# Optimization experiments

Hardware: AMD Instinct MI355X
Metric: run time of the kernel (lower is better)

Reference implementation:

```python
import jax, jax.numpy as jnp
import numpy as np

N = 100_000   # nodes
E = 1_250_000 # edges
D = 64        # feature dim


def setup_inputs() -> dict:
    key = jax.random.key(0)
    k1, k2, k3, k4 = jax.random.split(key, 4)
    x = jax.random.normal(k1, (N, D), dtype=jnp.float32)
    edge_index = jax.random.randint(k2, (2, E), 0, N, dtype=jnp.int32)
    s = 1.0 / np.sqrt(D)  # glorot-ish scale
    W1 = jax.random.uniform(k3, (D, D), minval=-s, maxval=s, dtype=jnp.float32)
    W2 = jax.random.uniform(k4, (D, D), minval=-s, maxval=s, dtype=jnp.float32)
    b1 = jnp.zeros((D,), jnp.float32)
    b2 = jnp.zeros((D,), jnp.float32)
    return {"x": x, "edge_index": edge_index, "W1": W1, "b1": b1, "W2": W2, "b2": b2}


def gcn_conv(x, edge_index, W, b):
    # PyG GCNConv: add self-loops, symmetric normalization D^-1/2 A D^-1/2,
    # linear transform, scatter-add aggregation over destination nodes.
    n = x.shape[0]
    src, dst = edge_index[0], edge_index[1]
    xw = x @ W  # [N, D]
    deg = jax.ops.segment_sum(jnp.ones((edge_index.shape[1],), x.dtype), dst,
                              num_segments=n) + 1.0  # +1 for self-loop
    inv_sqrt = jax.lax.rsqrt(deg)  # [N]
    coef = inv_sqrt[src] * inv_sqrt[dst]  # [E]
    agg = jax.ops.segment_sum(xw[src] * coef[:, None], dst, num_segments=n)
    # self-loop contribution: coef_ii = deg_i^-1
    agg = agg + xw * (inv_sqrt * inv_sqrt)[:, None]
    return agg + b


def reference(x, edge_index, W1, b1, W2, b2):
    h = jax.nn.relu(gcn_conv(x, edge_index, W1, b1))
    # dropout p=0.6 is identity in eval mode (training=False)
    out = gcn_conv(h, edge_index, W2, b2)
    return jax.nn.log_softmax(out, axis=1)
```

## Files before the change

kernel.cpp:

```cpp
#include <hip/hip_runtime.h>

#define DD 64
#define BSH 8
#define NB_MAX 512
#define SCAP 4096
#define BIN_CH 4096

typedef __attribute__((ext_vector_type(8))) short bf16x8;
typedef __attribute__((ext_vector_type(4))) float f32x4;
union Frag { bf16x8 v; uint32_t d[4]; };

__device__ __forceinline__ float bf_lo(uint32_t d) { return __uint_as_float(d << 16); }
__device__ __forceinline__ float bf_hi(uint32_t d) { return __uint_as_float(d & 0xffff0000u); }
__device__ __forceinline__ float bf2f(uint32_t h) { return __uint_as_float(h << 16); }
__device__ __forceinline__ uint32_t f2bf(float f) {
    uint32_t u = __float_as_uint(f);
    u += 0x7fffu + ((u >> 16) & 1u);
    return u >> 16;
}

__global__ __launch_bounds__(256) void bin_kernel(const int* __restrict__ src,
                                                  const int* __restrict__ dst,
                                                  int* __restrict__ bcnt,
                                                  uint32_t* __restrict__ staging,
                                                  int E, int NB) {
    __shared__ uint32_t cnt[NB_MAX];
    __shared__ uint32_t resv[NB_MAX];
    __shared__ uint16_t rk[BIN_CH];
    int tid = threadIdx.x;
    int base = blockIdx.x * BIN_CH;
    for (int b = tid; b < NB; b += 256) cnt[b] = 0;
    __syncthreads();
    for (int k = tid; k < BIN_CH; k += 256) {
        int g = base + k;
        if (g < E) {
            int b = dst[g] >> BSH;
            rk[k] = (uint16_t)atomicAdd(&cnt[b], 1u);
        }
    }
    __syncthreads();
    for (int b = tid; b < NB; b += 256) {
        uint32_t c = cnt[b];
        resv[b] = c ? (uint32_t)atomicAdd(&bcnt[b], (int)c) : 0u;
    }
    __syncthreads();
    for (int k = tid; k < BIN_CH; k += 256) {
        int g = base + k;
        if (g < E) {
            int s = src[g], d = dst[g];
            int b = d >> BSH;
            uint32_t pos = resv[b] + rk[k];
            if (pos < SCAP)
                staging[(size_t)b * SCAP + pos] = ((uint32_t)s << BSH) | (uint32_t)(d & ((1 << BSH) - 1));
        }
    }
}

__global__ __launch_bounds__(256) void sort_kernel(const int* __restrict__ bcnt,
                                                   const uint32_t* __restrict__ staging,
                                                   int* __restrict__ rowptr,
                                                   float* __restrict__ inv,
                                                   uint32_t* __restrict__ srcs,
                                                   int n, int E, int NB) {
    __shared__ uint32_t raw[SCAP];
    __shared__ uint32_t sorted[SCAP];
    __shared__ int scnt[1 << BSH];
    __shared__ int soff[1 << BSH];
    __shared__ int lcur[1 << BSH];
    __shared__ int red[256];
    int tid = threadIdx.x;
    int b = blockIdx.x;
    int base = b << BSH;
    int nd = min(1 << BSH, n - base);
    int cb = min(bcnt[b], SCAP);

    int part = 0;
    for (int j = tid; j < b; j += 256) part += bcnt[j];
    red[tid] = part;
    __syncthreads();
    for (int o = 128; o > 0; o >>= 1) {
        if (tid < o) red[tid] += red[tid + o];
        __syncthreads();
    }
    int bbase = red[0];

    scnt[tid] = 0;
    if (tid < ((1 << BSH) - 256)) {}
    __syncthreads();
    for (int k = tid; k < cb; k += 256) {
        uint32_t w = staging[(size_t)b * SCAP + k];
        raw[k] = w;
        atomicAdd(&scnt[w & ((1 << BSH) - 1)], 1);
    }
    __syncthreads();
    int v = scnt[tid];
    red[tid] = v;
    __syncthreads();
    for (int o = 1; o < 256; o <<= 1) {
        int t = (tid >= o) ? red[tid - o] : 0;
        __syncthreads();
        red[tid] += t;
        __syncthreads();
    }
    soff[tid] = red[tid] - v;
    lcur[tid] = red[tid] - v;
    if (tid < nd) {
        rowptr[base + tid] = bbase + soff[tid];
        inv[base + tid] = rsqrtf((float)v + 1.0f);
    }
    if (b == NB - 1 && tid == 0) rowptr[n] = E;
    __syncthreads();
    for (int k = tid; k < cb; k += 256) {
        uint32_t w = raw[k];
        int p = atomicAdd(&lcur[w & ((1 << BSH) - 1)], 1);
        sorted[p] = w >> BSH;
    }
    __syncthreads();
    for (int k = tid; k < cb; k += 256) srcs[bbase + k] = sorted[k];
}

template <int XBF>
__global__ __launch_bounds__(256) void gemm64_mfma(const void* __restrict__ Xv,
                                                   const float* __restrict__ W,
                                                   uint16_t* __restrict__ Y, int n) {
    __shared__ float Ws[DD * DD];
    int tid = threadIdx.x;
    for (int i = tid; i < DD * DD; i += 256) Ws[i] = W[i];
    __syncthreads();
    int lane = tid & 63, quad = lane >> 4, l16 = lane & 15;

    Frag bhi[4][2], blo[4][2];
#pragma unroll
    for (int t = 0; t < 4; ++t)
#pragma unroll
        for (int c = 0; c < 2; ++c) {
            int col = t * 16 + l16;
            int kb = c * 32 + quad * 8;
#pragma unroll
            for (int i = 0; i < 4; ++i) {
                float w0 = Ws[(kb + 2 * i) * DD + col];
                float w1 = Ws[(kb + 2 * i + 1) * DD + col];
                uint32_t h0 = f2bf(w0), h1 = f2bf(w1);
                uint32_t l0 = f2bf(w0 - bf2f(h0)), l1 = f2bf(w1 - bf2f(h1));
                bhi[t][c].d[i] = h0 | (h1 << 16);
                blo[t][c].d[i] = l0 | (l1 << 16);
            }
        }

    int ngroups = (n + 15) >> 4;
    int nwaves = gridDim.x * 4;
    int wid = blockIdx.x * 4 + (tid >> 6);
    for (int g = wid; g < ngroups; g += nwaves) {
        int rb = g << 4;
        int row = min(rb + l16, n - 1);
        f32x4 acc[4];
#pragma unroll
        for (int t = 0; t < 4; ++t) acc[t] = (f32x4){0.f, 0.f, 0.f, 0.f};
#pragma unroll
        for (int c = 0; c < 2; ++c) {
            Frag ahi, alo;
            if constexpr (XBF == 0) {
                const float* xr = (const float*)Xv + (size_t)row * DD + c * 32 + quad * 8;
                float4 x0 = *(const float4*)xr;
                float4 x1 = *(const float4*)(xr + 4);
                float f[8] = {x0.x, x0.y, x0.z, x0.w, x1.x, x1.y, x1.z, x1.w};
#pragma unroll
                for (int i = 0; i < 4; ++i) {
                    uint32_t h0 = f2bf(f[2 * i]), h1 = f2bf(f[2 * i + 1]);
                    ahi.d[i] = h0 | (h1 << 16);
                    alo.d[i] = f2bf(f[2 * i] - bf2f(h0)) | (f2bf(f[2 * i + 1] - bf2f(h1)) << 16);
                }
            } else {
                const int4* xr = (const int4*)((const uint32_t*)Xv + (size_t)row * 32 + c * 16 + quad * 4);
                int4 a = *xr;
                ahi.d[0] = a.x; ahi.d[1] = a.y; ahi.d[2] = a.z; ahi.d[3] = a.w;
            }
#pragma unroll
            for (int t = 0; t < 4; ++t) {
                acc[t] = __builtin_amdgcn_mfma_f32_16x16x32_bf16(ahi.v, bhi[t][c].v, acc[t], 0, 0, 0);
                acc[t] = __builtin_amdgcn_mfma_f32_16x16x32_bf16(ahi.v, blo[t][c].v, acc[t], 0, 0, 0);
                if constexpr (XBF == 0)
                    acc[t] = __builtin_amdgcn_mfma_f32_16x16x32_bf16(alo.v, bhi[t][c].v, acc[t], 0, 0, 0);
            }
        }
#pragma unroll
        for (int t = 0; t < 4; ++t)
#pragma unroll
            for (int r = 0; r < 4; ++r) {
                int ro = rb + quad * 4 + r;
                if (ro < n) Y[(size_t)ro * DD + t * 16 + l16] = (uint16_t)f2bf(acc[t][r]);
            }
    }
}

template <int MODE>
__global__ __launch_bounds__(256) void agg_kernel(const int* __restrict__ rowptr,
                                                  const uint32_t* __restrict__ srcs,
                                                  const float* __restrict__ inv,
                                                  const uint32_t* __restrict__ XWb,
                                                  const float* __restrict__ b,
                                                  void* __restrict__ OUTv, int n) {
    int gid = blockIdx.x * 256 + threadIdx.x;
    int i = gid >> 6, lane = gid & 63;
    if (i >= n) return;
    int q = lane >> 4, m = lane & 15;

    float iv = inv[i];
    float a0 = 0.f, a1 = 0.f, a2 = 0.f, a3 = 0.f;
    if (q == 0) {
        float iv2 = iv * iv;
        int2 d = *(const int2*)(XWb + (size_t)i * 32 + 2 * m);
        float4 bb = *(const float4*)(b + 4 * m);
        a0 = fmaf(bf_lo((uint32_t)d.x), iv2, bb.x);
        a1 = fmaf(bf_hi((uint32_t)d.x), iv2, bb.y);
        a2 = fmaf(bf_lo((uint32_t)d.y), iv2, bb.z);
        a3 = fmaf(bf_hi((uint32_t)d.y), iv2, bb.w);
    }

    int jstart = rowptr[i], jend = rowptr[i + 1];
    if (jstart < jend) {
        int last = jend - 1;
        int jq = jstart + q;
        uint32_t s0 = srcs[min(jq, last)];
        uint32_t s1 = srcs[min(jq + 4, last)];
        uint32_t s2 = srcs[min(jq + 8, last)];
        float v0 = inv[s0], v1 = inv[s1];
        int2 d0 = *(const int2*)(XWb + (size_t)s0 * 32 + 2 * m);
        int2 d1 = *(const int2*)(XWb + (size_t)s1 * 32 + 2 * m);
        for (int j = jq; j < jend; j += 4) {
            uint32_t s3 = srcs[min(j + 12, last)];
            float v2 = inv[s2];
            int2 d2 = *(const int2*)(XWb + (size_t)s2 * 32 + 2 * m);
            float c = v0 * iv;
            a0 = fmaf(bf_lo((uint32_t)d0.x), c, a0);
            a1 = fmaf(bf_hi((uint32_t)d0.x), c, a1);
            a2 = fmaf(bf_lo((uint32_t)d0.y), c, a2);
            a3 = fmaf(bf_hi((uint32_t)d0.y), c, a3);
            s0 = s1; s1 = s2; s2 = s3;
            v0 = v1; v1 = v2;
            d0 = d1; d1 = d2;
        }
    }

    a0 += __shfl_xor(a0, 32, 64); a0 += __shfl_xor(a0, 16, 64);
    a1 += __shfl_xor(a1, 32, 64); a1 += __shfl_xor(a1, 16, 64);
    a2 += __shfl_xor(a2, 32, 64); a2 += __shfl_xor(a2, 16, 64);
    a3 += __shfl_xor(a3, 32, 64); a3 += __shfl_xor(a3, 16, 64);

    if (MODE == 0) {
        if (q == 0) {
            int2 d;
            d.x = (int)((f2bf(fmaxf(a1, 0.f)) << 16) | f2bf(fmaxf(a0, 0.f)));
            d.y = (int)((f2bf(fmaxf(a3, 0.f)) << 16) | f2bf(fmaxf(a2, 0.f)));
            *(int2*)((uint32_t*)OUTv + (size_t)i * 32 + 2 * m) = d;
        }
    } else {
        float mx = fmaxf(fmaxf(a0, a1), fmaxf(a2, a3));
#pragma unroll
        for (int o = 8; o > 0; o >>= 1) mx = fmaxf(mx, __shfl_xor(mx, o, 64));
        float e = __expf(a0 - mx) + __expf(a1 - mx) + __expf(a2 - mx) + __expf(a3 - mx);
#pragma unroll
        for (int o = 8; o > 0; o >>= 1) e += __shfl_xor(e, o, 64);
        float ls = __logf(e);
        if (q == 0) {
            float4 r = make_float4(a0 - mx - ls, a1 - mx - ls, a2 - mx - ls, a3 - mx - ls);
            *(float4*)((float*)OUTv + (size_t)i * DD + 4 * m) = r;
        }
    }
}

extern "C" void kernel_launch(void* const* d_in, const int* in_sizes, int n_in,
                              void* d_out, int out_size, void* d_ws, size_t ws_size,
                              hipStream_t stream) {
    const float* x  = (const float*)d_in[0];
    const int*   ei = (const int*)d_in[1];
    const float* W1 = (const float*)d_in[2];
    const float* b1 = (const float*)d_in[3];
    const float* W2 = (const float*)d_in[4];
    const float* b2 = (const float*)d_in[5];
    float* out = (float*)d_out;

    const int n = in_sizes[0] / DD;
    const int E = in_sizes[1] / 2;
    const int* src = ei;
    const int* dst = ei + E;
    const int NB = (n + (1 << BSH) - 1) >> BSH;

    size_t off = 0;
    int* base = (int*)d_ws;
    int* bcnt = base + off; off += NB_MAX;
    uint32_t* staging = (uint32_t*)(base + off); off += (size_t)NB_MAX * SCAP;
    uint32_t* srcs = (uint32_t*)(base + off); off += E;
    int* rowptr = base + off; off += (size_t)n + 1;
    float* inv  = (float*)(base + off); off += n;
    uint32_t* XWb = (uint32_t*)(base + off); off += (size_t)n * 32;
    uint32_t* hb  = (uint32_t*)(base + off); off += (size_t)n * 32;

    hipMemsetAsync(bcnt, 0, NB_MAX * sizeof(int), stream);
    bin_kernel<<<(E + BIN_CH - 1) / BIN_CH, 256, 0, stream>>>(src, dst, bcnt, staging, E, NB);
    sort_kernel<<<NB, 256, 0, stream>>>(bcnt, staging, rowptr, inv, srcs, n, E, NB);

    gemm64_mfma<0><<<1024, 256, 0, stream>>>(x, W1, (uint16_t*)XWb, n);
    agg_kernel<0><<<(n * DD + 255) / 256, 256, 0, stream>>>(rowptr, srcs, inv, XWb, b1, hb, n);

    gemm64_mfma<1><<<1024, 256, 0, stream>>>(hb, W2, (uint16_t*)XWb, n);
    agg_kernel<1><<<(n * DD + 255) / 256, 256, 0, stream>>>(rowptr, srcs, inv, XWb, b2, out, n);
}
```

Before: 263.6 us.

## Fuse all GCN stages into one cooperative persistent kernel with precomputed edge coefficients

Replaces the memset plus six separate launches with a single cooperative kernel that runs binning, per-bucket sorting, coefficient precomputation, both GEMMs and both aggregations, separated by grid-wide syncs. It adds a pass that stores each edge as a (src, inv[src]*inv[dst]) record, so the aggregation loops no longer gather inv per neighbour. Aggregation becomes a persistent grid-stride loop over nodes. The aim is to cut launch overhead and inter-kernel gaps and to remove the dependent inv gather, at the cost of grid-sync overhead, reduced parallelism in the bin and sort phases, and a larger edge array in memory.

```diff
diff --git a/kernel.cpp b/kernel.cpp
--- a/kernel.cpp
+++ b/kernel.cpp
@@ -1,4 +1,7 @@
 #include <hip/hip_runtime.h>
+#include <hip/hip_cooperative_groups.h>
+
+namespace cg = cooperative_groups;
 
 #define DD 64
 #define BSH 8
@@ -19,111 +22,15 @@
     return u >> 16;
 }
 
-__global__ __launch_bounds__(256) void bin_kernel(const int* __restrict__ src,
-                                                  const int* __restrict__ dst,
-                                                  int* __restrict__ bcnt,
-                                                  uint32_t* __restrict__ staging,
-                                                  int E, int NB) {
-    __shared__ uint32_t cnt[NB_MAX];
-    __shared__ uint32_t resv[NB_MAX];
-    __shared__ uint16_t rk[BIN_CH];
-    int tid = threadIdx.x;
-    int base = blockIdx.x * BIN_CH;
-    for (int b = tid; b < NB; b += 256) cnt[b] = 0;
-    __syncthreads();
-    for (int k = tid; k < BIN_CH; k += 256) {
-        int g = base + k;
-        if (g < E) {
-            int b = dst[g] >> BSH;
-            rk[k] = (uint16_t)atomicAdd(&cnt[b], 1u);
-        }
-    }
-    __syncthreads();
-    for (int b = tid; b < NB; b += 256) {
-        uint32_t c = cnt[b];
-        resv[b] = c ? (uint32_t)atomicAdd(&bcnt[b], (int)c) : 0u;
-    }
-    __syncthreads();
-    for (int k = tid; k < BIN_CH; k += 256) {
-        int g = base + k;
-        if (g < E) {
-            int s = src[g], d = dst[g];
-            int b = d >> BSH;
-            uint32_t pos = resv[b] + rk[k];
-            if (pos < SCAP)
-                staging[(size_t)b * SCAP + pos] = ((uint32_t)s << BSH) | (uint32_t)(d & ((1 << BSH) - 1));
-        }
-    }
-}
-
-__global__ __launch_bounds__(256) void sort_kernel(const int* __restrict__ bcnt,
-                                                   const uint32_t* __restrict__ staging,
-                                                   int* __restrict__ rowptr,
-                                                   float* __restrict__ inv,
-                                                   uint32_t* __restrict__ srcs,
-                                                   int n, int E, int NB) {
-    __shared__ uint32_t raw[SCAP];
-    __shared__ uint32_t sorted[SCAP];
-    __shared__ int scnt[1 << BSH];
-    __shared__ int soff[1 << BSH];
-    __shared__ int lcur[1 << BSH];
-    __shared__ int red[256];
-    int tid = threadIdx.x;
-    int b = blockIdx.x;
-    int base = b << BSH;
-    int nd = min(1 << BSH, n - base);
-    int cb = min(bcnt[b], SCAP);
-
-    int part = 0;
-    for (int j = tid; j < b; j += 256) part += bcnt[j];
-    red[tid] = part;
-    __syncthreads();
-    for (int o = 128; o > 0; o >>= 1) {
-        if (tid < o) red[tid] += red[tid + o];
-        __syncthreads();
-    }
-    int bbase = red[0];
-
-    scnt[tid] = 0;
-    if (tid < ((1 << BSH) - 256)) {}
-    __syncthreads();
-    for (int k = tid; k < cb; k += 256) {
-        uint32_t w = staging[(size_t)b * SCAP + k];
-        raw[k] = w;
-        atomicAdd(&scnt[w & ((1 << BSH) - 1)], 1);
-    }
-    __syncthreads();
-    int v = scnt[tid];
-    red[tid] = v;
-    __syncthreads();
-    for (int o = 1; o < 256; o <<= 1) {
-        int t = (tid >= o) ? red[tid - o] : 0;
-        __syncthreads();
-        red[tid] += t;
-        __syncthreads();
-    }
-    soff[tid] = red[tid] - v;
-    lcur[tid] = red[tid] - v;
-    if (tid < nd) {
-        rowptr[base + tid] = bbase + soff[tid];
-        inv[base + tid] = rsqrtf((float)v + 1.0f);
-    }
-    if (b == NB - 1 && tid == 0) rowptr[n] = E;
-    __syncthreads();
-    for (int k = tid; k < cb; k += 256) {
-        uint32_t w = raw[k];
-        int p = atomicAdd(&lcur[w & ((1 << BSH) - 1)], 1);
-        sorted[p] = w >> BSH;
-    }
-    __syncthreads();
-    for (int k = tid; k < cb; k += 256) srcs[bbase + k] = sorted[k];
-}
+struct SBin  { uint32_t cnt[NB_MAX]; uint32_t resv[NB_MAX]; uint16_t rk[BIN_CH]; };
+struct SSort { uint32_t raw[SCAP]; int scnt[1 << BSH]; int red[256]; };
+struct SGemm { float Ws[DD * DD]; };
+union SMem { SBin bin; SSort sort; SGemm gemm; };
 
 template <int XBF>
-__global__ __launch_bounds__(256) void gemm64_mfma(const void* __restrict__ Xv,
-                                                   const float* __restrict__ W,
-                                                   uint16_t* __restrict__ Y, int n) {
-    __shared__ float Ws[DD * DD];
+__device__ __forceinline__ void gemm_body(float* Ws, const void* __restrict__ Xv,
+                                          const float* __restrict__ W,
+                                          uint16_t* __restrict__ Y, int n) {
     int tid = threadIdx.x;
     for (int i = tid; i < DD * DD; i += 256) Ws[i] = W[i];
     __syncthreads();
@@ -194,79 +101,199 @@
 }
 
 template <int MODE>
-__global__ __launch_bounds__(256) void agg_kernel(const int* __restrict__ rowptr,
-                                                  const uint32_t* __restrict__ srcs,
-                                                  const float* __restrict__ inv,
-                                                  const uint32_t* __restrict__ XWb,
-                                                  const float* __restrict__ b,
-                                                  void* __restrict__ OUTv, int n) {
-    int gid = blockIdx.x * 256 + threadIdx.x;
-    int i = gid >> 6, lane = gid & 63;
-    if (i >= n) return;
-    int q = lane >> 4, m = lane & 15;
-
-    float iv = inv[i];
-    float a0 = 0.f, a1 = 0.f, a2 = 0.f, a3 = 0.f;
-    if (q == 0) {
-        float iv2 = iv * iv;
-        int2 d = *(const int2*)(XWb + (size_t)i * 32 + 2 * m);
-        float4 bb = *(const float4*)(b + 4 * m);
-        a0 = fmaf(bf_lo((uint32_t)d.x), iv2, bb.x);
-        a1 = fmaf(bf_hi((uint32_t)d.x), iv2, bb.y);
-        a2 = fmaf(bf_lo((uint32_t)d.y), iv2, bb.z);
-        a3 = fmaf(bf_hi((uint32_t)d.y), iv2, bb.w);
-    }
-
-    int jstart = rowptr[i], jend = rowptr[i + 1];
-    if (jstart < jend) {
-        int last = jend - 1;
-        int jq = jstart + q;
-        uint32_t s0 = srcs[min(jq, last)];
-        uint32_t s1 = srcs[min(jq + 4, last)];
-        uint32_t s2 = srcs[min(jq + 8, last)];
-        float v0 = inv[s0], v1 = inv[s1];
-        int2 d0 = *(const int2*)(XWb + (size_t)s0 * 32 + 2 * m);
-        int2 d1 = *(const int2*)(XWb + (size_t)s1 * 32 + 2 * m);
-        for (int j = jq; j < jend; j += 4) {
-            uint32_t s3 = srcs[min(j + 12, last)];
-            float v2 = inv[s2];
-            int2 d2 = *(const int2*)(XWb + (size_t)s2 * 32 + 2 * m);
-            float c = v0 * iv;
-            a0 = fmaf(bf_lo((uint32_t)d0.x), c, a0);
-            a1 = fmaf(bf_hi((uint32_t)d0.x), c, a1);
-            a2 = fmaf(bf_lo((uint32_t)d0.y), c, a2);
-            a3 = fmaf(bf_hi((uint32_t)d0.y), c, a3);
-            s0 = s1; s1 = s2; s2 = s3;
-            v0 = v1; v1 = v2;
-            d0 = d1; d1 = d2;
-        }
-    }
-
-    a0 += __shfl_xor(a0, 32, 64); a0 += __shfl_xor(a0, 16, 64);
-    a1 += __shfl_xor(a1, 32, 64); a1 += __shfl_xor(a1, 16, 64);
-    a2 += __shfl_xor(a2, 32, 64); a2 += __shfl_xor(a2, 16, 64);
-    a3 += __shfl_xor(a3, 32, 64); a3 += __shfl_xor(a3, 16, 64);
-
-    if (MODE == 0) {
+__device__ __forceinline__ void agg_body(const int* __restrict__ rowptr,
+                                         const int2* __restrict__ recs,
+                                         const float* __restrict__ inv,
+                                         const uint32_t* __restrict__ XWb,
+                                         const float* __restrict__ b,
+                                         void* __restrict__ OUTv, int n) {
+    int tid = threadIdx.x;
+    int lane = tid & 63, q = lane >> 4, m = lane & 15;
+    int wave0 = (blockIdx.x * 256 + tid) >> 6;
+    int nwaves = gridDim.x * 4;
+    for (int i = wave0; i < n; i += nwaves) {
+        float a0 = 0.f, a1 = 0.f, a2 = 0.f, a3 = 0.f;
         if (q == 0) {
-            int2 d;
-            d.x = (int)((f2bf(fmaxf(a1, 0.f)) << 16) | f2bf(fmaxf(a0, 0.f)));
-            d.y = (int)((f2bf(fmaxf(a3, 0.f)) << 16) | f2bf(fmaxf(a2, 0.f)));
-            *(int2*)((uint32_t*)OUTv + (size_t)i * 32 + 2 * m) = d;
-        }
-    } else {
-        float mx = fmaxf(fmaxf(a0, a1), fmaxf(a2, a3));
-#pragma unroll
-        for (int o = 8; o > 0; o >>= 1) mx = fmaxf(mx, __shfl_xor(mx, o, 64));
-        float e = __expf(a0 - mx) + __expf(a1 - mx) + __expf(a2 - mx) + __expf(a3 - mx);
-#pragma unroll
-        for (int o = 8; o > 0; o >>= 1) e += __shfl_xor(e, o, 64);
-        float ls = __logf(e);
-        if (q == 0) {
-            float4 r = make_float4(a0 - mx - ls, a1 - mx - ls, a2 - mx - ls, a3 - mx - ls);
-            *(float4*)((float*)OUTv + (size_t)i * DD + 4 * m) = r;
-        }
-    }
+            float iv = inv[i];
+            float iv2 = iv * iv;
+            int2 d = *(const int2*)(XWb + (size_t)i * 32 + 2 * m);
+            float4 bb = *(const float4*)(b + 4 * m);
+            a0 = fmaf(bf_lo((uint32_t)d.x), iv2, bb.x);
+            a1 = fmaf(bf_hi((uint32_t)d.x), iv2, bb.y);
+            a2 = fmaf(bf_lo((uint32_t)d.y), iv2, bb.z);
+            a3 = fmaf(bf_hi((uint32_t)d.y), iv2, bb.w);
+        }
+        int jstart = rowptr[i], jend = rowptr[i + 1];
+        if (jstart < jend) {
+            int last = jend - 1;
+            int jq = jstart + q;
+            int2 r0 = recs[min(jq, last)];
+            int2 r1 = recs[min(jq + 4, last)];
+            int2 r2 = recs[min(jq + 8, last)];
+            int2 d0 = *(const int2*)(XWb + (size_t)r0.x * 32 + 2 * m);
+            int2 d1 = *(const int2*)(XWb + (size_t)r1.x * 32 + 2 * m);
+            for (int j = jq; j < jend; j += 4) {
+                int2 r3 = recs[min(j + 12, last)];
+                int2 d2 = *(const int2*)(XWb + (size_t)r2.x * 32 + 2 * m);
+                float c = __int_as_float(r0.y);
+                a0 = fmaf(bf_lo((uint32_t)d0.x), c, a0);
+                a1 = fmaf(bf_hi((uint32_t)d0.x), c, a1);
+                a2 = fmaf(bf_lo((uint32_t)d0.y), c, a2);
+                a3 = fmaf(bf_hi((uint32_t)d0.y), c, a3);
+                r0 = r1; r1 = r2; r2 = r3;
+                d0 = d1; d1 = d2;
+            }
+        }
+        a0 += __shfl_xor(a0, 32, 64); a0 += __shfl_xor(a0, 16, 64);
+        a1 += __shfl_xor(a1, 32, 64); a1 += __shfl_xor(a1, 16, 64);
+        a2 += __shfl_xor(a2, 32, 64); a2 += __shfl_xor(a2, 16, 64);
+        a3 += __shfl_xor(a3, 32, 64); a3 += __shfl_xor(a3, 16, 64);
+        if (MODE == 0) {
+            if (q == 0) {
+                int2 d;
+                d.x = (int)((f2bf(fmaxf(a1, 0.f)) << 16) | f2bf(fmaxf(a0, 0.f)));
+                d.y = (int)((f2bf(fmaxf(a3, 0.f)) << 16) | f2bf(fmaxf(a2, 0.f)));
+                *(int2*)((uint32_t*)OUTv + (size_t)i * 32 + 2 * m) = d;
+            }
+        } else {
+            float mx = fmaxf(fmaxf(a0, a1), fmaxf(a2, a3));
+#pragma unroll
+            for (int o = 8; o > 0; o >>= 1) mx = fmaxf(mx, __shfl_xor(mx, o, 64));
+            float e = __expf(a0 - mx) + __expf(a1 - mx) + __expf(a2 - mx) + __expf(a3 - mx);
+#pragma unroll
+            for (int o = 8; o > 0; o >>= 1) e += __shfl_xor(e, o, 64);
+            float ls = __logf(e);
+            if (q == 0) {
+                float4 r = make_float4(a0 - mx - ls, a1 - mx - ls, a2 - mx - ls, a3 - mx - ls);
+                *(float4*)((float*)OUTv + (size_t)i * DD + 4 * m) = r;
+            }
+        }
+    }
+}
+
+__global__ __launch_bounds__(256, 4) void mega_kernel(
+    const float* __restrict__ x, const int* __restrict__ esrc, const int* __restrict__ edst,
+    const float* __restrict__ W1, const float* __restrict__ b1,
+    const float* __restrict__ W2, const float* __restrict__ b2,
+    float* __restrict__ out, int n, int E, int NB,
+    int* __restrict__ bcnt, uint32_t* __restrict__ staging, uint32_t* __restrict__ packed,
+    int* __restrict__ rowptr, float* __restrict__ inv, int2* __restrict__ recs,
+    uint32_t* __restrict__ XWb, uint32_t* __restrict__ hb) {
+    cg::grid_group grid = cg::this_grid();
+    __shared__ SMem sm;
+    int tid = threadIdx.x;
+    int gtid = blockIdx.x * 256 + tid;
+    int gtotal = gridDim.x * 256;
+
+    for (int k = gtid; k < NB_MAX; k += gtotal) bcnt[k] = 0;
+    grid.sync();
+
+    int nchunks = (E + BIN_CH - 1) / BIN_CH;
+    for (int chunk = blockIdx.x; chunk < nchunks; chunk += gridDim.x) {
+        int base = chunk * BIN_CH;
+        __syncthreads();
+        for (int b = tid; b < NB; b += 256) sm.bin.cnt[b] = 0;
+        __syncthreads();
+        for (int k = tid; k < BIN_CH; k += 256) {
+            int g = base + k;
+            if (g < E) {
+                int b = edst[g] >> BSH;
+                sm.bin.rk[k] = (uint16_t)atomicAdd(&sm.bin.cnt[b], 1u);
+            }
+        }
+        __syncthreads();
+        for (int b = tid; b < NB; b += 256) {
+            uint32_t c = sm.bin.cnt[b];
+            sm.bin.resv[b] = c ? (uint32_t)atomicAdd(&bcnt[b], (int)c) : 0u;
+        }
+        __syncthreads();
+        for (int k = tid; k < BIN_CH; k += 256) {
+            int g = base + k;
+            if (g < E) {
+                int s = esrc[g], d = edst[g];
+                int b = d >> BSH;
+                uint32_t pos = sm.bin.resv[b] + sm.bin.rk[k];
+                if (pos < SCAP)
+                    staging[(size_t)b * SCAP + pos] =
+                        ((uint32_t)s << BSH) | (uint32_t)(d & ((1 << BSH) - 1));
+            }
+        }
+    }
+    grid.sync();
+
+    for (int b = blockIdx.x; b < NB; b += gridDim.x) {
+        int base = b << BSH;
+        int nd = min(1 << BSH, n - base);
+        int cb = min(bcnt[b], SCAP);
+        __syncthreads();
+        int part = 0;
+        for (int j = tid; j < b; j += 256) part += bcnt[j];
+        sm.sort.red[tid] = part;
+        __syncthreads();
+        for (int o = 128; o > 0; o >>= 1) {
+            if (tid < o) sm.sort.red[tid] += sm.sort.red[tid + o];
+            __syncthreads();
+        }
+        int bbase = sm.sort.red[0];
+        __syncthreads();
+        sm.sort.scnt[tid] = 0;
+        __syncthreads();
+        for (int k = tid; k < cb; k += 256) {
+            uint32_t w = staging[(size_t)b * SCAP + k];
+            sm.sort.raw[k] = w;
+            atomicAdd(&sm.sort.scnt[w & ((1 << BSH) - 1)], 1);
+        }
+        __syncthreads();
+        int v = sm.sort.scnt[tid];
+        sm.sort.red[tid] = v;
+        __syncthreads();
+        for (int o = 1; o < 256; o <<= 1) {
+            int t = (tid >= o) ? sm.sort.red[tid - o] : 0;
+            __syncthreads();
+            sm.sort.red[tid] += t;
+            __syncthreads();
+        }
+        int excl = sm.sort.red[tid] - v;
+        sm.sort.scnt[tid] = excl;
+        if (tid < nd) {
+            rowptr[base + tid] = bbase + excl;
+            inv[base + tid] = rsqrtf((float)v + 1.0f);
+        }
+        if (b == NB - 1 && tid == 0) rowptr[n] = E;
+        __syncthreads();
+        for (int k = tid; k < cb; k += 256) {
+            uint32_t w = sm.sort.raw[k];
+            int p = atomicAdd(&sm.sort.scnt[w & ((1 << BSH) - 1)], 1);
+            packed[bbase + p] = w;
+        }
+    }
+    grid.sync();
+
+    for (int b = blockIdx.x; b < NB; b += gridDim.x) {
+        int base = b << BSH;
+        int nd = min(1 << BSH, n - base);
+        int s0 = rowptr[base], e0 = rowptr[base + nd];
+        for (int k = s0 + tid; k < e0; k += 256) {
+            uint32_t w = packed[k];
+            int s = (int)(w >> BSH);
+            int2 r;
+            r.x = s;
+            r.y = __float_as_int(inv[s] * inv[base + (int)(w & ((1 << BSH) - 1))]);
+            recs[k] = r;
+        }
+    }
+    grid.sync();
+
+    gemm_body<0>(sm.gemm.Ws, x, W1, (uint16_t*)XWb, n);
+    grid.sync();
+
+    agg_body<0>(rowptr, recs, inv, XWb, b1, hb, n);
+    grid.sync();
+
+    gemm_body<1>(sm.gemm.Ws, hb, W2, (uint16_t*)XWb, n);
+    grid.sync();
+
+    agg_body<1>(rowptr, recs, inv, XWb, b2, out, n);
 }
 
 extern "C" void kernel_launch(void* const* d_in, const int* in_sizes, int n_in,
@@ -280,29 +307,30 @@
     const float* b2 = (const float*)d_in[5];
     float* out = (float*)d_out;
 
-    const int n = in_sizes[0] / DD;
-    const int E = in_sizes[1] / 2;
-    const int* src = ei;
-    const int* dst = ei + E;
-    const int NB = (n + (1 << BSH) - 1) >> BSH;
+    int n = in_sizes[0] / DD;
+    int E = in_sizes[1] / 2;
+    const int* esrc = ei;
+    const int* edst = ei + E;
+    int NB = (n + (1 << BSH) - 1) >> BSH;
 
     size_t off = 0;
     int* base = (int*)d_ws;
     int* bcnt = base + off; off += NB_MAX;
     uint32_t* staging = (uint32_t*)(base + off); off += (size_t)NB_MAX * SCAP;
-    uint32_t* srcs = (uint32_t*)(base + off); off += E;
+    uint32_t* packed  = (uint32_t*)(base + off); off += E;
     int* rowptr = base + off; off += (size_t)n + 1;
     float* inv  = (float*)(base + off); off += n;
+    off = (off + 1) & ~(size_t)1;
+    int2* recs  = (int2*)(base + off); off += (size_t)2 * E;
     uint32_t* XWb = (uint32_t*)(base + off); off += (size_t)n * 32;
     uint32_t* hb  = (uint32_t*)(base + off); off += (size_t)n * 32;
 
-    hipMemsetAsync(bcnt, 0, NB_MAX * sizeof(int), stream);
-    bin_kernel<<<(E + BIN_CH - 1) / BIN_CH, 256, 0, stream>>>(src, dst, bcnt, staging, E, NB);
-    sort_kernel<<<NB, 256, 0, stream>>>(bcnt, staging, rowptr, inv, srcs, n, E, NB);
-
-    gemm64_mfma<0><<<1024, 256, 0, stream>>>(x, W1, (uint16_t*)XWb, n);
-    agg_kernel<0><<<(n * DD + 255) / 256, 256, 0, stream>>>(rowptr, srcs, inv, XWb, b1, hb, n);
-
-    gemm64_mfma<1><<<1024, 256, 0, stream>>>(hb, W2, (uint16_t*)XWb, n);
-    agg_kernel<1><<<(n * DD + 255) / 256, 256, 0, stream>>>(rowptr, srcs, inv, XWb, b2, out, n);
-}
+    int perCU = 0;
+    hipOccupancyMaxActiveBlocksPerMultiprocessor(&perCU, mega_kernel, 256, 0);
+    if (perCU < 1) perCU = 1;
+    int G = perCU * 256;
+
+    void* args[] = {&x, &esrc, &edst, &W1, &b1, &W2, &b2, &out, &n, &E, &NB,
+                    &bcnt, &staging, &packed, &rowptr, &inv, &recs, &XWb, &hb};
+    hipLaunchCooperativeKernel((void*)mega_kernel, dim3(G), dim3(256), args, 0, stream);
+}
```

After: 817.5 us. +210.2%, slower.
